# Optimization experiments

Measured on AMD Instinct MI355X. Metric: run time of the kernel, lower is better.

Reference implementation:

```python
import jax, jax.numpy as jnp
import numpy as np

EPS = 1e-8  # torch F.cosine_similarity default eps


def _angleproto_loss(x, w, b):
    # x: [N, 2, D]
    pos = x[:, 0, :]     # [N, D] positives (rows of sim matrix)
    anc = x[:, 1, :]     # [N, D] anchors   (cols of sim matrix)
    # cosine similarity via normalize + GEMM (avoids O(N^2 D) broadcast)
    pos_n = pos / jnp.maximum(jnp.linalg.norm(pos, axis=-1, keepdims=True), EPS)
    anc_n = anc / jnp.maximum(jnp.linalg.norm(anc, axis=-1, keepdims=True), EPS)
    logits = jnp.einsum('nd,md->nm', pos_n, anc_n)  # [N, N]
    # NOTE: original torch.clamp(self.w, 1e-6) is not in-place -> no-op; keep w as-is.
    logits = logits * w + b
    # cross-entropy with labels = arange(N): mean of -log_softmax diagonal
    logp = jax.nn.log_softmax(logits, axis=-1)
    n = x.shape[0]
    loss = -jnp.mean(jnp.diagonal(logp))
    return loss


def setup_inputs() -> dict:
    key = jax.random.key(0)
    k1, = jax.random.split(key, 1)
    N, D = 8192, 192
    x = jax.random.normal(k1, (N, 2, D), dtype=jnp.float32)
    w = jnp.asarray(10.0, dtype=jnp.float32)
    b = jnp.asarray(-5.0, dtype=jnp.float32)
    return {"x": x, "w": w, "b": b}


def reference(x, w, b):
    return _angleproto_loss(x, w, b)
```

## Files before the change

kernel.cpp:

```cpp
#include <hip/hip_runtime.h>
#include <hip/hip_bf16.h>

#define N 8192
#define D 192
#define NCHUNK 16
#define CHUNK_COLS 512
#define TILE_COLS 64
#define NTILES (CHUNK_COLS / TILE_COLS)
#define BLOCK_ROWS 256
#define FRAG_BYTES 1024
#define TILE_BYTES ((TILE_COLS / 16) * 6 * FRAG_BYTES)

typedef short short8 __attribute__((ext_vector_type(8)));
typedef float f32x4 __attribute__((ext_vector_type(4)));

#define GLOAD16(gptr, lptr)                                                               \
  __builtin_amdgcn_global_load_lds((const __attribute__((address_space(1))) void*)(gptr), \
                                   (__attribute__((address_space(3))) void*)(lptr), 16, 0, 0)

__global__ __launch_bounds__(256) void norm_kernel(
    const float* __restrict__ x,
    const float* __restrict__ wp,
    __hip_bfloat16* __restrict__ posn,
    __hip_bfloat16* __restrict__ ancn,
    float* __restrict__ diag) {
  const float c1 = (*wp) * 1.4426950408889634f;
  int gw = (int)((blockIdx.x * 256 + threadIdx.x) >> 6);
  int lane = threadIdx.x & 63;
  if (gw >= N) return;
  const float* row = x + (size_t)gw * (2 * D);
  float p[3], a[3];
  float ssp = 0.f, ssa = 0.f, dt = 0.f;
#pragma unroll
  for (int j = 0; j < 3; ++j) {
    p[j] = row[lane + 64 * j];
    a[j] = row[D + lane + 64 * j];
    ssp += p[j] * p[j];
    ssa += a[j] * a[j];
    dt += p[j] * a[j];
  }
#pragma unroll
  for (int off = 32; off >= 1; off >>= 1) {
    ssp += __shfl_xor(ssp, off, 64);
    ssa += __shfl_xor(ssa, off, 64);
    dt += __shfl_xor(dt, off, 64);
  }
  float invp = 1.f / fmaxf(sqrtf(ssp), 1e-8f);
  float inva = 1.f / fmaxf(sqrtf(ssa), 1e-8f);
#pragma unroll
  for (int j = 0; j < 3; ++j) {
    posn[(size_t)gw * D + lane + 64 * j] = __float2bfloat16(p[j] * invp * c1);
    ancn[(size_t)gw * D + lane + 64 * j] = __float2bfloat16(a[j] * inva);
  }
  if (lane == 0) diag[gw] = dt * invp * inva;
}

__global__ __launch_bounds__(256) __attribute__((amdgpu_waves_per_eu(2, 2)))
void gemm_lse_kernel(
    const __hip_bfloat16* __restrict__ posn,
    const __hip_bfloat16* __restrict__ ancn,
    const float* __restrict__ wp,
    float* __restrict__ partial) {
  __shared__ char lds[2 * TILE_BYTES];

  const int lane = (int)(threadIdx.x & 63);
  const int wv = (int)(threadIdx.x >> 6);
  const int chunk = (int)(blockIdx.x & (NCHUNK - 1));
  const int rb = (int)(blockIdx.x >> 4);
  const int rowBase = rb * BLOCK_ROWS + wv * 64;
  const int colBase = chunk * CHUNK_COLS;

  const float c0 = -fabsf(*wp) * 1.4426950408889634f;

  const int r15 = lane & 15;
  const int khi = (lane >> 4) * 8;

  short8 af[4][6];
#pragma unroll
  for (int rs = 0; rs < 4; ++rs)
#pragma unroll
    for (int ks = 0; ks < 6; ++ks)
      af[rs][ks] = *(const short8*)(posn + (size_t)(rowBase + rs * 16 + r15) * D + ks * 32 + khi);

  auto stage = [&](int buf, int t) {
    const __hip_bfloat16* g =
        ancn + (size_t)(colBase + t * TILE_COLS + wv * 16 + r15) * D + khi;
    char* l = lds + buf * TILE_BYTES + wv * 6 * FRAG_BYTES;
#pragma unroll
    for (int ks = 0; ks < 6; ++ks) GLOAD16(g + ks * 32, l + ks * FRAG_BYTES);
  };

  stage(0, 0);
  __syncthreads();

  float s[4][4];
#pragma unroll
  for (int rs = 0; rs < 4; ++rs)
#pragma unroll
    for (int r = 0; r < 4; ++r) s[rs][r] = 0.f;

  for (int t = 0; t < NTILES; ++t) {
    if (t + 1 < NTILES) stage((t + 1) & 1, t + 1);
    const char* buf = lds + (t & 1) * TILE_BYTES;
#pragma unroll
    for (int ct = 0; ct < TILE_COLS / 16; ++ct) {
      f32x4 acc[4];
#pragma unroll
      for (int rs = 0; rs < 4; ++rs) acc[rs] = (f32x4){c0, c0, c0, c0};
#pragma unroll
      for (int ks = 0; ks < 6; ++ks) {
        short8 bfk = *(const short8*)(buf + (ct * 6 + ks) * FRAG_BYTES + lane * 16);
#pragma unroll
        for (int rs = 0; rs < 4; ++rs)
          acc[rs] = __builtin_amdgcn_mfma_f32_16x16x32_bf16(af[rs][ks], bfk, acc[rs], 0, 0, 0);
      }
#pragma unroll
      for (int rs = 0; rs < 4; ++rs)
#pragma unroll
        for (int r = 0; r < 4; ++r)
          s[rs][r] += __builtin_amdgcn_exp2f(acc[rs][r]);
    }
    __syncthreads();
  }

#pragma unroll
  for (int off = 1; off < 16; off <<= 1)
#pragma unroll
    for (int rs = 0; rs < 4; ++rs)
#pragma unroll
      for (int r = 0; r < 4; ++r) s[rs][r] += __shfl_xor(s[rs][r], off, 64);

  if (r15 == 0) {
    const int rgrp = (lane >> 4) * 4;
#pragma unroll
    for (int rs = 0; rs < 4; ++rs)
#pragma unroll
      for (int r = 0; r < 4; ++r)
        partial[(size_t)chunk * N + rowBase + rs * 16 + rgrp + r] = s[rs][r];
  }
}

__global__ __launch_bounds__(256) void finalize1_kernel(
    const float* __restrict__ partial,
    const float* __restrict__ diag,
    const float* __restrict__ wp,
    const float* __restrict__ bp,
    float* __restrict__ blocksum) {
  const float w = *wp, b = *bp;
  const float M = fabsf(w) + b;
  int i = (int)(blockIdx.x * 256 + threadIdx.x);
  float s = 0.f;
#pragma unroll
  for (int c = 0; c < NCHUNK; ++c) s += partial[(size_t)c * N + i];
  float acc = fmaf(diag[i], w, b) - (M + logf(s));
#pragma unroll
  for (int off = 32; off >= 1; off >>= 1) acc += __shfl_xor(acc, off, 64);
  __shared__ float red[4];
  if ((threadIdx.x & 63) == 0) red[threadIdx.x >> 6] = acc;
  __syncthreads();
  if (threadIdx.x == 0) blocksum[blockIdx.x] = red[0] + red[1] + red[2] + red[3];
}

__global__ __launch_bounds__(64) void finalize2_kernel(
    const float* __restrict__ blocksum, float* __restrict__ out) {
  int lane = (int)threadIdx.x;
  float v = (lane < 32) ? blocksum[lane] : 0.f;
#pragma unroll
  for (int off = 32; off >= 1; off >>= 1) v += __shfl_xor(v, off, 64);
  if (lane == 0) out[0] = -v / (float)N;
}

extern "C" void kernel_launch(void* const* d_in, const int* in_sizes, int n_in,
                              void* d_out, int out_size, void* d_ws, size_t ws_size,
                              hipStream_t stream) {
  const float* x = (const float*)d_in[0];
  const float* wp = (const float*)d_in[1];
  const float* bp = (const float*)d_in[2];
  float* out = (float*)d_out;

  char* ws = (char*)d_ws;
  __hip_bfloat16* posn = (__hip_bfloat16*)ws;
  __hip_bfloat16* ancn = (__hip_bfloat16*)(ws + 3145728);
  float* diag = (float*)(ws + 6291456);
  float* partial = (float*)(ws + 6324224);
  float* blocksum = (float*)(ws + 6848512);

  norm_kernel<<<N / 4, 256, 0, stream>>>(x, wp, posn, ancn, diag);
  gemm_lse_kernel<<<(N / BLOCK_ROWS) * NCHUNK, 256, 0, stream>>>(posn, ancn, wp, partial);
  finalize1_kernel<<<N / 256, 256, 0, stream>>>(partial, diag, wp, bp, blocksum);
  finalize2_kernel<<<1, 64, 0, stream>>>(blocksum, out);
}
```

Baseline: 43.60 us.

## Use smaller column chunks with single-shot LDS staging instead of double buffering

The GEMM+LSE kernel now takes 128-column chunks instead of 512, giving 2048 blocks instead of 512. Each block loads its whole 128-column anchor tile into LDS once, overlapped with the A-fragment register loads, and drops the double-buffered tile loop and its per-tile barriers. This adds parallelism and removes sync overhead. The cost is that each block re-reads its 256 rows of A-fragments for a quarter as much work, and the partial buffer and finalize reduction grow from 16 to 64 chunks.

```diff
diff --git a/kernel.cpp b/kernel.cpp
--- a/kernel.cpp
+++ b/kernel.cpp
@@ -3,13 +3,11 @@
 
 #define N 8192
 #define D 192
-#define NCHUNK 16
-#define CHUNK_COLS 512
-#define TILE_COLS 64
-#define NTILES (CHUNK_COLS / TILE_COLS)
-#define BLOCK_ROWS 256
+#define BROWS 256
+#define BCOLS 128
+#define NCCHUNK (N / BCOLS)
 #define FRAG_BYTES 1024
-#define TILE_BYTES ((TILE_COLS / 16) * 6 * FRAG_BYTES)
+#define NFRAGS ((BCOLS / 16) * 6)
 
 typedef short short8 __attribute__((ext_vector_type(8)));
 typedef float f32x4 __attribute__((ext_vector_type(4)));
@@ -61,19 +59,27 @@
     const __hip_bfloat16* __restrict__ ancn,
     const float* __restrict__ wp,
     float* __restrict__ partial) {
-  __shared__ char lds[2 * TILE_BYTES];
+  __shared__ char lds[NFRAGS * FRAG_BYTES];
 
   const int lane = (int)(threadIdx.x & 63);
   const int wv = (int)(threadIdx.x >> 6);
-  const int chunk = (int)(blockIdx.x & (NCHUNK - 1));
-  const int rb = (int)(blockIdx.x >> 4);
-  const int rowBase = rb * BLOCK_ROWS + wv * 64;
-  const int colBase = chunk * CHUNK_COLS;
+  const int cchunk = (int)(blockIdx.x & (NCCHUNK - 1));
+  const int rb = (int)(blockIdx.x >> 6);
+  const int rowBase = rb * BROWS + wv * 64;
+  const int colBase = cchunk * BCOLS;
 
   const float c0 = -fabsf(*wp) * 1.4426950408889634f;
 
   const int r15 = lane & 15;
   const int khi = (lane >> 4) * 8;
+
+#pragma unroll
+  for (int j = 0; j < 12; ++j) {
+    const int ct = wv * 2 + (j / 6);
+    const int ks = j % 6;
+    const __hip_bfloat16* g = ancn + (size_t)(colBase + ct * 16 + r15) * D + ks * 32 + khi;
+    GLOAD16(g, lds + (ct * 6 + ks) * FRAG_BYTES);
+  }
 
   short8 af[4][6];
 #pragma unroll
@@ -82,45 +88,31 @@
     for (int ks = 0; ks < 6; ++ks)
       af[rs][ks] = *(const short8*)(posn + (size_t)(rowBase + rs * 16 + r15) * D + ks * 32 + khi);
 
-  auto stage = [&](int buf, int t) {
-    const __hip_bfloat16* g =
-        ancn + (size_t)(colBase + t * TILE_COLS + wv * 16 + r15) * D + khi;
-    char* l = lds + buf * TILE_BYTES + wv * 6 * FRAG_BYTES;
-#pragma unroll
-    for (int ks = 0; ks < 6; ++ks) GLOAD16(g + ks * 32, l + ks * FRAG_BYTES);
-  };
-
-  stage(0, 0);
-  __syncthreads();
-
   float s[4][4];
 #pragma unroll
   for (int rs = 0; rs < 4; ++rs)
 #pragma unroll
     for (int r = 0; r < 4; ++r) s[rs][r] = 0.f;
 
-  for (int t = 0; t < NTILES; ++t) {
-    if (t + 1 < NTILES) stage((t + 1) & 1, t + 1);
-    const char* buf = lds + (t & 1) * TILE_BYTES;
+  __syncthreads();
+
+#pragma unroll 2
+  for (int ct = 0; ct < BCOLS / 16; ++ct) {
+    f32x4 acc[4];
 #pragma unroll
-    for (int ct = 0; ct < TILE_COLS / 16; ++ct) {
-      f32x4 acc[4];
+    for (int rs = 0; rs < 4; ++rs) acc[rs] = (f32x4){c0, c0, c0, c0};
 #pragma unroll
-      for (int rs = 0; rs < 4; ++rs) acc[rs] = (f32x4){c0, c0, c0, c0};
-#pragma unroll
-      for (int ks = 0; ks < 6; ++ks) {
-        short8 bfk = *(const short8*)(buf + (ct * 6 + ks) * FRAG_BYTES + lane * 16);
-#pragma unroll
-        for (int rs = 0; rs < 4; ++rs)
-          acc[rs] = __builtin_amdgcn_mfma_f32_16x16x32_bf16(af[rs][ks], bfk, acc[rs], 0, 0, 0);
-      }
+    for (int ks = 0; ks < 6; ++ks) {
+      short8 bfk = *(const short8*)(lds + (ct * 6 + ks) * FRAG_BYTES + lane * 16);
 #pragma unroll
       for (int rs = 0; rs < 4; ++rs)
+        acc[rs] = __builtin_amdgcn_mfma_f32_16x16x32_bf16(af[rs][ks], bfk, acc[rs], 0, 0, 0);
+    }
 #pragma unroll
-        for (int r = 0; r < 4; ++r)
-          s[rs][r] += __builtin_amdgcn_exp2f(acc[rs][r]);
-    }
-    __syncthreads();
+    for (int rs = 0; rs < 4; ++rs)
+#pragma unroll
+      for (int r = 0; r < 4; ++r)
+        s[rs][r] += __builtin_amdgcn_exp2f(acc[rs][r]);
   }
 
 #pragma unroll
@@ -136,7 +128,7 @@
     for (int rs = 0; rs < 4; ++rs)
 #pragma unroll
       for (int r = 0; r < 4; ++r)
-        partial[(size_t)chunk * N + rowBase + rs * 16 + rgrp + r] = s[rs][r];
+        partial[(size_t)cchunk * N + rowBase + rs * 16 + rgrp + r] = s[rs][r];
   }
 }
 
@@ -151,7 +143,7 @@
   int i = (int)(blockIdx.x * 256 + threadIdx.x);
   float s = 0.f;
 #pragma unroll
-  for (int c = 0; c < NCHUNK; ++c) s += partial[(size_t)c * N + i];
+  for (int c = 0; c < NCCHUNK; ++c) s += partial[(size_t)c * N + i];
   float acc = fmaf(diag[i], w, b) - (M + logf(s));
 #pragma unroll
   for (int off = 32; off >= 1; off >>= 1) acc += __shfl_xor(acc, off, 64);
@@ -183,10 +175,10 @@
   __hip_bfloat16* ancn = (__hip_bfloat16*)(ws + 3145728);
   float* diag = (float*)(ws + 6291456);
   float* partial = (float*)(ws + 6324224);
-  float* blocksum = (float*)(ws + 6848512);
+  float* blocksum = (float*)(ws + 8421376);
 
   norm_kernel<<<N / 4, 256, 0, stream>>>(x, wp, posn, ancn, diag);
-  gemm_lse_kernel<<<(N / BLOCK_ROWS) * NCHUNK, 256, 0, stream>>>(posn, ancn, wp, partial);
+  gemm_lse_kernel<<<(N / BROWS) * NCCHUNK, 256, 0, stream>>>(posn, ancn, wp, partial);
   finalize1_kernel<<<N / 256, 256, 0, stream>>>(partial, diag, wp, bp, blocksum);
   finalize2_kernel<<<1, 64, 0, stream>>>(blocksum, out);
 }
```

New measurement: 71.69 us. 64.4% more time.

## Retile GEMM-LSE into 256x128 output tiles with K-streamed A and B

Applied to the files above, without the earlier changes.

Replaces the old scheme, where each wave kept its positive rows resident in registers and streamed 512-column chunks, with classic 256x128 output tiles. Both A and B fragments are now staged through double-buffered LDS across six K phases, and a swizzled block index is meant to improve L2 reuse. The aim is more parallelism (2048 blocks instead of 512) and better operand reuse per MFMA. In exchange, the partial-sum buffer grows to 128 column slices per row, which adds finalize reads and workspace, and the waves_per_eu hint is dropped.

```diff
diff --git a/kernel.cpp b/kernel.cpp
--- a/kernel.cpp
+++ b/kernel.cpp
@@ -3,13 +3,15 @@
 
 #define N 8192
 #define D 192
-#define NCHUNK 16
-#define CHUNK_COLS 512
-#define TILE_COLS 64
-#define NTILES (CHUNK_COLS / TILE_COLS)
-#define BLOCK_ROWS 256
-#define FRAG_BYTES 1024
-#define TILE_BYTES ((TILE_COLS / 16) * 6 * FRAG_BYTES)
+#define BM 256
+#define BN 128
+#define BK 32
+#define NKP (D / BK)
+#define NCB (N / BN)
+#define FRAG 1024
+#define AFRAGS (BM / 16)
+#define BFRAGS (BN / 16)
+#define PHASE_BYTES ((AFRAGS + BFRAGS) * FRAG)
 
 typedef short short8 __attribute__((ext_vector_type(8)));
 typedef float f32x4 __attribute__((ext_vector_type(4)));
@@ -55,88 +57,96 @@
   if (lane == 0) diag[gw] = dt * invp * inva;
 }
 
-__global__ __launch_bounds__(256) __attribute__((amdgpu_waves_per_eu(2, 2)))
-void gemm_lse_kernel(
+__global__ __launch_bounds__(256) void gemm_lse_kernel(
     const __hip_bfloat16* __restrict__ posn,
     const __hip_bfloat16* __restrict__ ancn,
     const float* __restrict__ wp,
     float* __restrict__ partial) {
-  __shared__ char lds[2 * TILE_BYTES];
+  __shared__ char lds[2 * PHASE_BYTES];
 
   const int lane = (int)(threadIdx.x & 63);
   const int wv = (int)(threadIdx.x >> 6);
-  const int chunk = (int)(blockIdx.x & (NCHUNK - 1));
-  const int rb = (int)(blockIdx.x >> 4);
-  const int rowBase = rb * BLOCK_ROWS + wv * 64;
-  const int colBase = chunk * CHUNK_COLS;
+  const int sw = (int)((blockIdx.x & 7) * 256 + (blockIdx.x >> 3));
+  const int cb = sw & (NCB - 1);
+  const int rb = sw >> 6;
+  const int rowBase0 = rb * BM;
+  const int colBase0 = cb * BN;
+  const int wr = wv >> 1;
+  const int wc = wv & 1;
 
   const float c0 = -fabsf(*wp) * 1.4426950408889634f;
 
   const int r15 = lane & 15;
   const int khi = (lane >> 4) * 8;
 
-  short8 af[4][6];
-#pragma unroll
-  for (int rs = 0; rs < 4; ++rs)
-#pragma unroll
-    for (int ks = 0; ks < 6; ++ks)
-      af[rs][ks] = *(const short8*)(posn + (size_t)(rowBase + rs * 16 + r15) * D + ks * 32 + khi);
-
-  auto stage = [&](int buf, int t) {
-    const __hip_bfloat16* g =
-        ancn + (size_t)(colBase + t * TILE_COLS + wv * 16 + r15) * D + khi;
-    char* l = lds + buf * TILE_BYTES + wv * 6 * FRAG_BYTES;
-#pragma unroll
-    for (int ks = 0; ks < 6; ++ks) GLOAD16(g + ks * 32, l + ks * FRAG_BYTES);
+  auto stage = [&](int buf, int p) {
+    const int kb = p * BK;
+    char* l = lds + buf * PHASE_BYTES;
+#pragma unroll
+    for (int j = 0; j < 6; ++j) {
+      const int f = wv * 6 + j;
+      const __hip_bfloat16* g =
+          (f < AFRAGS)
+              ? posn + (size_t)(rowBase0 + f * 16 + r15) * D + kb + khi
+              : ancn + (size_t)(colBase0 + (f - AFRAGS) * 16 + r15) * D + kb + khi;
+      GLOAD16(g, l + f * FRAG);
+    }
   };
+
+  f32x4 acc[8][4];
+#pragma unroll
+  for (int rs = 0; rs < 8; ++rs)
+#pragma unroll
+    for (int cs = 0; cs < 4; ++cs) acc[rs][cs] = (f32x4){c0, c0, c0, c0};
 
   stage(0, 0);
   __syncthreads();
 
-  float s[4][4];
-#pragma unroll
-  for (int rs = 0; rs < 4; ++rs)
-#pragma unroll
-    for (int r = 0; r < 4; ++r) s[rs][r] = 0.f;
-
-  for (int t = 0; t < NTILES; ++t) {
-    if (t + 1 < NTILES) stage((t + 1) & 1, t + 1);
-    const char* buf = lds + (t & 1) * TILE_BYTES;
-#pragma unroll
-    for (int ct = 0; ct < TILE_COLS / 16; ++ct) {
-      f32x4 acc[4];
-#pragma unroll
-      for (int rs = 0; rs < 4; ++rs) acc[rs] = (f32x4){c0, c0, c0, c0};
-#pragma unroll
-      for (int ks = 0; ks < 6; ++ks) {
-        short8 bfk = *(const short8*)(buf + (ct * 6 + ks) * FRAG_BYTES + lane * 16);
-#pragma unroll
-        for (int rs = 0; rs < 4; ++rs)
-          acc[rs] = __builtin_amdgcn_mfma_f32_16x16x32_bf16(af[rs][ks], bfk, acc[rs], 0, 0, 0);
-      }
-#pragma unroll
-      for (int rs = 0; rs < 4; ++rs)
-#pragma unroll
-        for (int r = 0; r < 4; ++r)
-          s[rs][r] += __builtin_amdgcn_exp2f(acc[rs][r]);
+  for (int p = 0; p < NKP; ++p) {
+    if (p + 1 < NKP) stage((p + 1) & 1, p + 1);
+    const char* Ab = lds + (p & 1) * PHASE_BYTES;
+    const char* Bb = Ab + AFRAGS * FRAG;
+    short8 af[8];
+#pragma unroll
+    for (int rs = 0; rs < 8; ++rs)
+      af[rs] = *(const short8*)(Ab + (wr * 8 + rs) * FRAG + lane * 16);
+#pragma unroll
+    for (int cs = 0; cs < 4; ++cs) {
+      short8 bf = *(const short8*)(Bb + (wc * 4 + cs) * FRAG + lane * 16);
+#pragma unroll
+      for (int rs = 0; rs < 8; ++rs)
+        acc[rs][cs] = __builtin_amdgcn_mfma_f32_16x16x32_bf16(af[rs], bf, acc[rs][cs], 0, 0, 0);
     }
     __syncthreads();
   }
 
+  float srow[8][4];
+#pragma unroll
+  for (int rs = 0; rs < 8; ++rs)
+#pragma unroll
+    for (int r = 0; r < 4; ++r) srow[rs][r] = 0.f;
+#pragma unroll
+  for (int rs = 0; rs < 8; ++rs)
+#pragma unroll
+    for (int cs = 0; cs < 4; ++cs)
+#pragma unroll
+      for (int r = 0; r < 4; ++r)
+        srow[rs][r] += __builtin_amdgcn_exp2f(acc[rs][cs][r]);
 #pragma unroll
   for (int off = 1; off < 16; off <<= 1)
 #pragma unroll
-    for (int rs = 0; rs < 4; ++rs)
-#pragma unroll
-      for (int r = 0; r < 4; ++r) s[rs][r] += __shfl_xor(s[rs][r], off, 64);
+    for (int rs = 0; rs < 8; ++rs)
+#pragma unroll
+      for (int r = 0; r < 4; ++r) srow[rs][r] += __shfl_xor(srow[rs][r], off, 64);
 
   if (r15 == 0) {
-    const int rgrp = (lane >> 4) * 4;
-#pragma unroll
-    for (int rs = 0; rs < 4; ++rs)
+    const int rg = (lane >> 4) * 4;
+#pragma unroll
+    for (int rs = 0; rs < 8; ++rs)
 #pragma unroll
       for (int r = 0; r < 4; ++r)
-        partial[(size_t)chunk * N + rowBase + rs * 16 + rgrp + r] = s[rs][r];
+        partial[(size_t)(cb * 2 + wc) * N + rowBase0 + wr * 128 + rs * 16 + rg + r] =
+            srow[rs][r];
   }
 }
 
@@ -151,7 +161,7 @@
   int i = (int)(blockIdx.x * 256 + threadIdx.x);
   float s = 0.f;
 #pragma unroll
-  for (int c = 0; c < NCHUNK; ++c) s += partial[(size_t)c * N + i];
+  for (int c = 0; c < 2 * NCB; ++c) s += partial[(size_t)c * N + i];
   float acc = fmaf(diag[i], w, b) - (M + logf(s));
 #pragma unroll
   for (int off = 32; off >= 1; off >>= 1) acc += __shfl_xor(acc, off, 64);
@@ -183,10 +193,10 @@
   __hip_bfloat16* ancn = (__hip_bfloat16*)(ws + 3145728);
   float* diag = (float*)(ws + 6291456);
   float* partial = (float*)(ws + 6324224);
-  float* blocksum = (float*)(ws + 6848512);
+  float* blocksum = (float*)(ws + 10518528);
 
   norm_kernel<<<N / 4, 256, 0, stream>>>(x, wp, posn, ancn, diag);
-  gemm_lse_kernel<<<(N / BLOCK_ROWS) * NCHUNK, 256, 0, stream>>>(posn, ancn, wp, partial);
+  gemm_lse_kernel<<<(N / BM) * NCB, 256, 0, stream>>>(posn, ancn, wp, partial);
   finalize1_kernel<<<N / 256, 256, 0, stream>>>(partial, diag, wp, bp, blocksum);
   finalize2_kernel<<<1, 64, 0, stream>>>(blocksum, out);
 }
```

Result: slower. 110.6 us (+153.6%).
